# Kernel tuning notes

Hardware: AMD Instinct MI355X
Metric: run time of the kernel (lower is better)

Reference implementation:

```python
import jax, jax.numpy as jnp
import numpy as np

S, B, E, H, FFN = 2048, 2, 1024, 16, 4096
HD = E // H
EPS = 1e-5

def setup_inputs() -> dict:
    key = jax.random.key(0)
    ks = jax.random.split(key, 10)
    w = lambda k, shape: 0.02 * jax.random.normal(k, shape, dtype=jnp.float32)
    inp = {
        "x": jax.random.normal(ks[0], (S, B, E), dtype=jnp.float32),
        "key_padding_mask": jax.random.randint(ks[1], (B, S), 0, 2) == 1,
        # attention projections, stored as (in, out) so y = x @ W + b
        "Wq": w(ks[2], (E, E)), "bq": jnp.zeros((E,), jnp.float32),
        "Wk": w(ks[3], (E, E)), "bk": jnp.zeros((E,), jnp.float32),
        "Wv": w(ks[4], (E, E)), "bv": jnp.zeros((E,), jnp.float32),
        "Wo": w(ks[5], (E, E)), "bo": jnp.zeros((E,), jnp.float32),
        "ln1_g": jnp.ones((E,), jnp.float32), "ln1_b": jnp.zeros((E,), jnp.float32),
        "W1": w(ks[6], (E, FFN)), "b1": jnp.zeros((FFN,), jnp.float32),
        "W2": w(ks[7], (FFN, E)), "b2": jnp.zeros((E,), jnp.float32),
        "ln2_g": jnp.ones((E,), jnp.float32), "ln2_b": jnp.zeros((E,), jnp.float32),
    }
    return inp

def layer_norm(x, g, b):
    m = jnp.mean(x, axis=-1, keepdims=True)
    v = jnp.mean(jnp.square(x - m), axis=-1, keepdims=True)
    return (x - m) * jax.lax.rsqrt(v + EPS) * g + b

def reference(x, key_padding_mask, Wq, bq, Wk, bk, Wv, bv, Wo, bo,
              ln1_g, ln1_b, W1, b1, W2, b2, ln2_g, ln2_b):
    # ---- self-attention (post-LN, normalize_before=False) ----
    residual = x  # (S, B, E)
    scaling = 1.0 / jnp.sqrt(jnp.float32(HD))
    q = (scaling * (x @ Wq + bq)).reshape(S, B, H, HD)
    k = (x @ Wk + bk).reshape(S, B, H, HD)
    v = (x @ Wv + bv).reshape(S, B, H, HD)
    # scores: (B, H, S_q, S_k)
    attn = jnp.einsum('ibhd,jbhd->bhij', q, k)
    attn = jnp.where(key_padding_mask[:, None, None, :], -jnp.inf, attn)
    attn = jax.nn.softmax(attn, axis=-1)
    out = jnp.einsum('bhij,jbhd->ibhd', attn, v).reshape(S, B, E)
    h = out @ Wo + bo
    h = layer_norm(residual + h, ln1_g, ln1_b)
    # ---- FFN ----
    residual = h
    f = jax.nn.relu(h @ W1 + b1) @ W2 + b2
    h = layer_norm(residual + f, ln2_g, ln2_b)
    # torch clamps only when inf/nan appear; finite inputs here so no-op
    return h
```

## Files before the change

kernel.cpp:

```cpp
#include <hip/hip_runtime.h>
#include <hip/hip_bf16.h>

using u16 = unsigned short;
using u32 = unsigned int;

constexpr int S_LEN = 2048, BATCH = 2, EMB = 1024, NHEAD = 16, HDIM = 64, FFN_DIM = 4096;
constexpr int NTOK = S_LEN * BATCH;
constexpr int QKV_N = 3 * EMB;

typedef __attribute__((ext_vector_type(4))) float f32x4;
typedef __attribute__((ext_vector_type(8))) short short8;
typedef __attribute__((ext_vector_type(8))) __bf16 bf16x8;
typedef __attribute__((ext_vector_type(8))) u16 ushort8;
typedef __attribute__((ext_vector_type(4))) u16 u16x4;

typedef const __attribute__((address_space(1))) u16 gu16;
typedef __attribute__((address_space(3))) u16 lu16;

__device__ __forceinline__ u16 f2bf(float f) {
  u32 u = __builtin_bit_cast(u32, f);
  u32 r = u + 0x7fffu + ((u >> 16) & 1u);
  return (u16)(r >> 16);
}
__device__ __forceinline__ float bf2f(u16 u) {
  return __builtin_bit_cast(float, (u32)u << 16);
}

__device__ __forceinline__ f32x4 mfma16(short8 a, short8 b, f32x4 c) {
  return __builtin_amdgcn_mfma_f32_16x16x32_bf16(
      __builtin_bit_cast(bf16x8, a), __builtin_bit_cast(bf16x8, b), c, 0, 0, 0);
}

__device__ __forceinline__ void gload16(const u16* g, u16* l) {
  __builtin_amdgcn_global_load_lds((gu16*)g, (lu16*)l, 16, 0, 0);
}

__global__ __launch_bounds__(256) void k_cvt_bf16(const float* __restrict__ in,
                                                  u16* __restrict__ out, int n) {
  int i = (blockIdx.x * 256 + threadIdx.x) * 8;
  if (i >= n) return;
  float4 a = *(const float4*)(in + i);
  float4 b = *(const float4*)(in + i + 4);
  ushort8 o;
  o[0] = f2bf(a.x); o[1] = f2bf(a.y); o[2] = f2bf(a.z); o[3] = f2bf(a.w);
  o[4] = f2bf(b.x); o[5] = f2bf(b.y); o[6] = f2bf(b.z); o[7] = f2bf(b.w);
  *(ushort8*)(out + i) = o;
}

__global__ __launch_bounds__(256) void k_transpose_w(const float* __restrict__ in,
                                                     u16* __restrict__ out, int R, int C,
                                                     float scale) {
  __shared__ float t[32][33];
  int c0 = blockIdx.x * 32, r0 = blockIdx.y * 32;
  int tx = threadIdx.x & 31, ty = threadIdx.x >> 5;
#pragma unroll
  for (int i = 0; i < 4; ++i)
    t[ty + i * 8][tx] = in[(r0 + ty + i * 8) * C + c0 + tx];
  __syncthreads();
#pragma unroll
  for (int i = 0; i < 4; ++i)
    out[(c0 + ty + i * 8) * R + r0 + tx] = f2bf(t[tx][ty + i * 8] * scale);
}

__global__ void k_bias_cat(const float* __restrict__ bq, const float* __restrict__ bk,
                           const float* __restrict__ bv, float* __restrict__ bcat) {
  int i = blockIdx.x * 256 + threadIdx.x;
  float v = (i < 1024) ? bq[i] * 0.125f : (i < 2048 ? bk[i - 1024] : bv[i - 2048]);
  bcat[i] = v;
}

__global__ void k_transpose_v(const u16* __restrict__ qkvb, u16* __restrict__ vT) {
  __shared__ u16 t[64][65];
  int s0 = blockIdx.x * 64;
  int bh = blockIdx.y;
  int b = bh >> 4, h = bh & 15;
  int tx = threadIdx.x, ty = threadIdx.y;
#pragma unroll
  for (int i = 0; i < 16; ++i) {
    int s = i * 4 + ty;
    t[s][tx] = qkvb[((s0 + s) * BATCH + b) * QKV_N + 2048 + h * HDIM + tx];
  }
  __syncthreads();
#pragma unroll
  for (int i = 0; i < 16; ++i) {
    int d = i * 4 + ty;
    vT[(bh * HDIM + d) * S_LEN + s0 + tx] = t[tx][d];
  }
}

template <int NS, bool RELU>
__global__ __launch_bounds__(256, 4) void k_gemm128(
    const u16* __restrict__ A, const u16* __restrict__ Bt,
    const float* __restrict__ bias, u16* __restrict__ C,
    u16* __restrict__ P1, u16* __restrict__ P2, u16* __restrict__ P3,
    int M, int N, int K, int nbx) {
  __shared__ u16 As[2][128 * 32];
  __shared__ u16 Bs[2][128 * 32];
  int tid = threadIdx.x;
  int lane = tid & 63;
  int lm = lane & 15, lg = lane >> 4;
  int w = tid >> 6;
  int wm = w >> 1, wn = w & 1;

  int cpx = gridDim.x >> 3;
  int nw = (blockIdx.x & 7) * cpx + (blockIdx.x >> 3);
  int nb = gridDim.x / NS;
  int slice = nw / nb;
  int t0 = nw - slice * nb;
  int m0 = (t0 / nbx) * 128, n0 = (t0 % nbx) * 128;
  int klen = K / NS, koff = slice * klen;

  f32x4 z = {0.f, 0.f, 0.f, 0.f};
  f32x4 acc[4][4];
#pragma unroll
  for (int mi = 0; mi < 4; ++mi)
#pragma unroll
    for (int ni = 0; ni < 4; ++ni) acc[mi][ni] = z;

  const u16* aSrc[2];
  const u16* bSrc[2];
  int dOff[2];
#pragma unroll
  for (int i = 0; i < 2; ++i) {
    int ci = i * 256 + tid;
    int row = ci >> 2, ch = ci & 3;
    int sc = 8 * (ch ^ ((row >> 1) & 3));
    aSrc[i] = A + (m0 + row) * K + koff + sc;
    bSrc[i] = Bt + (n0 + row) * K + koff + sc;
    dOff[i] = ci * 8;
  }

  auto stage = [&](int buf, int k0) {
#pragma unroll
    for (int i = 0; i < 2; ++i) {
      gload16(aSrc[i] + k0, &As[buf][0] + dOff[i]);
      gload16(bSrc[i] + k0, &Bs[buf][0] + dOff[i]);
    }
  };

  int swz = (lm >> 1) & 3;
  int nkt = klen >> 5;
  stage(0, 0);
  __syncthreads();
  for (int t = 0; t < nkt; ++t) {
    int cur = t & 1;
    if (t + 1 < nkt) stage(cur ^ 1, (t + 1) << 5);
    const u16* Ab = &As[cur][0];
    const u16* Bb = &Bs[cur][0];
    __builtin_amdgcn_s_setprio(1);
    short8 bf[4];
#pragma unroll
    for (int ni = 0; ni < 4; ++ni) {
      int row = wn * 64 + ni * 16 + lm;
      bf[ni] = *(const short8*)(Bb + row * 32 + 8 * (lg ^ swz));
    }
#pragma unroll
    for (int mi = 0; mi < 4; ++mi) {
      int row = wm * 64 + mi * 16 + lm;
      short8 af = *(const short8*)(Ab + row * 32 + 8 * (lg ^ swz));
#pragma unroll
      for (int ni = 0; ni < 4; ++ni)
        acc[mi][ni] = mfma16(af, bf[ni], acc[mi][ni]);
    }
    __builtin_amdgcn_s_setprio(0);
    __syncthreads();
  }

  u16* Cout = C;
  if (NS > 1) Cout = (slice == 0) ? C : (slice == 1 ? P1 : (slice == 2 ? P2 : P3));
#pragma unroll
  for (int ni = 0; ni < 4; ++ni) {
    int c = n0 + wn * 64 + ni * 16 + lm;
    float bc = (NS == 1) ? bias[c] : 0.f;
#pragma unroll
    for (int mi = 0; mi < 4; ++mi) {
#pragma unroll
      for (int j = 0; j < 4; ++j) {
        int r = m0 + wm * 64 + mi * 16 + lg * 4 + j;
        float x = acc[mi][ni][j] + bc;
        if (RELU) x = fmaxf(x, 0.f);
        Cout[r * N + c] = f2bf(x);
      }
    }
  }
}

template <bool OUTB>
__global__ __launch_bounds__(256) void k_reduce_ln(
    const u16* __restrict__ P0, const u16* __restrict__ P1,
    const u16* __restrict__ P2, const u16* __restrict__ P3,
    const float* __restrict__ bias, const float* __restrict__ resid,
    const float* __restrict__ gam, const float* __restrict__ bet,
    float* __restrict__ outf, u16* __restrict__ outb) {
  int r = blockIdx.x;
  int tid = threadIdx.x;
  int c4 = tid * 4;
  int idx = r * EMB + c4;
  u16x4 a0 = *(const u16x4*)(P0 + idx);
  u16x4 a1 = *(const u16x4*)(P1 + idx);
  u16x4 a2 = *(const u16x4*)(P2 + idx);
  u16x4 a3 = *(const u16x4*)(P3 + idx);
  float4 bi = *(const float4*)(bias + c4);
  float4 rs = *(const float4*)(resid + idx);
  float4 v;
  v.x = bf2f(a0[0]) + bf2f(a1[0]) + bf2f(a2[0]) + bf2f(a3[0]) + bi.x + rs.x;
  v.y = bf2f(a0[1]) + bf2f(a1[1]) + bf2f(a2[1]) + bf2f(a3[1]) + bi.y + rs.y;
  v.z = bf2f(a0[2]) + bf2f(a1[2]) + bf2f(a2[2]) + bf2f(a3[2]) + bi.z + rs.z;
  v.w = bf2f(a0[3]) + bf2f(a1[3]) + bf2f(a2[3]) + bf2f(a3[3]) + bi.w + rs.w;
  float s = v.x + v.y + v.z + v.w;
  float ss = v.x * v.x + v.y * v.y + v.z * v.z + v.w * v.w;
#pragma unroll
  for (int off = 1; off < 64; off <<= 1) {
    s += __shfl_xor(s, off);
    ss += __shfl_xor(ss, off);
  }
  __shared__ float red[2][4];
  int w = tid >> 6, lane = tid & 63;
  if (lane == 0) { red[0][w] = s; red[1][w] = ss; }
  __syncthreads();
  s = red[0][0] + red[0][1] + red[0][2] + red[0][3];
  ss = red[1][0] + red[1][1] + red[1][2] + red[1][3];
  float mean = s * (1.f / EMB);
  float var = ss * (1.f / EMB) - mean * mean;
  float inv = rsqrtf(var + 1e-5f);
  float4 g = *(const float4*)(gam + c4);
  float4 be = *(const float4*)(bet + c4);
  float4 o;
  o.x = (v.x - mean) * inv * g.x + be.x;
  o.y = (v.y - mean) * inv * g.y + be.y;
  o.z = (v.z - mean) * inv * g.z + be.z;
  o.w = (v.w - mean) * inv * g.w + be.w;
  *(float4*)(outf + idx) = o;
  if (OUTB) {
    u16 ob[4] = {f2bf(o.x), f2bf(o.y), f2bf(o.z), f2bf(o.w)};
    *(u16x4*)(outb + idx) = *(u16x4*)ob;
  }
}

__global__ __launch_bounds__(256) void k_attn(
    const u16* __restrict__ qkvb, const u16* __restrict__ vT,
    const int* __restrict__ mask, u16* __restrict__ outb) {
  __shared__ u16 Kl[2][4096];
  __shared__ u16 Vl[2][4096];
  __shared__ u16 Pl[4][1024];
  int tid = threadIdx.x;
  int lane = tid & 63, w = tid >> 6;
  int lm = lane & 15, lg = lane >> 4;
  int L = blockIdx.x;
  int bh = (L & 7) + 8 * (L >> 8);
  int qi0 = ((L >> 3) & 31) * 64;
  int b = bh >> 4, h = bh & 15;

  int qs = qi0 + w * 16 + lm;
  const u16* qp = qkvb + (qs * BATCH + b) * QKV_N + h * HDIM;
  short8 qf0 = *(const short8*)(qp + lg * 8);
  short8 qf1 = *(const short8*)(qp + 32 + lg * 8);

  int r0 = tid >> 3, c8 = tid & 7;
  int swz8 = 8 * (c8 ^ (r0 & 7));
  const u16* kA = qkvb + (r0 * BATCH + b) * QKV_N + 1024 + h * HDIM + swz8;
  const u16* kB = qkvb + ((r0 + 32) * BATCH + b) * QKV_N + 1024 + h * HDIM + swz8;
  const u16* vA = vT + (bh * HDIM + r0) * S_LEN + swz8;
  const u16* vB = vT + (bh * HDIM + r0 + 32) * S_LEN + swz8;
  const int KSTEP = 64 * BATCH * QKV_N;

  const int* mp = mask + b * S_LEN;

  u16* Pw = Pl[w];
  int rd_swz = (lm & 7) << 3;
  const u16* prd0 = Pw + lm * 64 + ((lg * 8) ^ rd_swz);
  const u16* prd1 = Pw + lm * 64 + ((32 + lg * 8) ^ rd_swz);
  int wbase[4], wswz[4];
#pragma unroll
  for (int j = 0; j < 4; ++j) {
    int row = lg * 4 + j;
    wbase[j] = row * 64;
    wswz[j] = (row & 7) << 3;
  }

  f32x4 z = {0.f, 0.f, 0.f, 0.f};
  f32x4 o[4] = {z, z, z, z};
  float lrow[4] = {0.f, 0.f, 0.f, 0.f};
  int mk[4], mknext[4];

  {
    u16* kd = Kl[0] + w * 512;
    u16* vd = Vl[0] + w * 512;
    gload16(kA, kd); gload16(kB, kd + 2048);
    gload16(vA, vd); gload16(vB, vd + 2048);
    kA += KSTEP; kB += KSTEP; vA += 64; vB += 64;
#pragma unroll
    for (int ni = 0; ni < 4; ++ni) mk[ni] = mp[ni * 16 + lm];
  }
  __syncthreads();

  int cur = 0;
  for (int kt = 0; kt < S_LEN; kt += 64) {
    if (kt + 64 < S_LEN) {
      u16* kd = Kl[cur ^ 1] + w * 512;
      u16* vd = Vl[cur ^ 1] + w * 512;
      gload16(kA, kd); gload16(kB, kd + 2048);
      gload16(vA, vd); gload16(vB, vd + 2048);
      kA += KSTEP; kB += KSTEP; vA += 64; vB += 64;
#pragma unroll
      for (int ni = 0; ni < 4; ++ni) mknext[ni] = mp[kt + 64 + ni * 16 + lm];
    }
    const u16* Kc = Kl[cur];
    const u16* Vc = Vl[cur];
#pragma unroll
    for (int ni = 0; ni < 4; ++ni) {
      const u16* kl = Kc + (ni * 16 + lm) * 64;
      short8 k0 = *(const short8*)(kl + ((lg * 8) ^ rd_swz));
      short8 k1 = *(const short8*)(kl + ((32 + lg * 8) ^ rd_swz));
      f32x4 t = mfma16(qf0, k0, z);
      f32x4 sv = mfma16(qf1, k1, t);
      float mb = mk[ni] ? -1e30f : 0.f;
      int csw = ni * 16 + lm;
#pragma unroll
      for (int j = 0; j < 4; ++j) {
        float p = __expf(fminf(sv[j] + mb, 30.f));
        lrow[j] += p;
        Pw[wbase[j] + (csw ^ wswz[j])] = f2bf(p);
      }
    }
    short8 pa0 = *(const short8*)prd0;
    short8 pa1 = *(const short8*)prd1;
#pragma unroll
    for (int ni = 0; ni < 4; ++ni) {
      const u16* vl = Vc + (ni * 16 + lm) * 64;
      short8 v0 = *(const short8*)(vl + ((lg * 8) ^ rd_swz));
      short8 v1 = *(const short8*)(vl + ((32 + lg * 8) ^ rd_swz));
      o[ni] = mfma16(pa0, v0, o[ni]);
      o[ni] = mfma16(pa1, v1, o[ni]);
    }
#pragma unroll
    for (int ni = 0; ni < 4; ++ni) mk[ni] = mknext[ni];
    __syncthreads();
    cur ^= 1;
  }

#pragma unroll
  for (int j = 0; j < 4; ++j) {
    float rs = lrow[j];
    rs += __shfl_xor(rs, 1);
    rs += __shfl_xor(rs, 2);
    rs += __shfl_xor(rs, 4);
    rs += __shfl_xor(rs, 8);
    lrow[j] = 1.f / rs;
  }
#pragma unroll
  for (int ni = 0; ni < 4; ++ni) {
    int c = h * HDIM + ni * 16 + lm;
#pragma unroll
    for (int j = 0; j < 4; ++j) {
      int srow = qi0 + w * 16 + lg * 4 + j;
      outb[(srow * BATCH + b) * EMB + c] = f2bf(o[ni][j] * lrow[j]);
    }
  }
}

extern "C" void kernel_launch(void* const* d_in, const int* in_sizes, int n_in,
                              void* d_out, int out_size, void* d_ws, size_t ws_size,
                              hipStream_t stream) {
  (void)in_sizes; (void)n_in; (void)out_size; (void)ws_size;
  const float* x = (const float*)d_in[0];
  const int* mask = (const int*)d_in[1];
  const float* Wq = (const float*)d_in[2];
  const float* bq = (const float*)d_in[3];
  const float* Wk = (const float*)d_in[4];
  const float* bk = (const float*)d_in[5];
  const float* Wv = (const float*)d_in[6];
  const float* bv = (const float*)d_in[7];
  const float* Wo = (const float*)d_in[8];
  const float* bo = (const float*)d_in[9];
  const float* g1 = (const float*)d_in[10];
  const float* be1 = (const float*)d_in[11];
  const float* W1 = (const float*)d_in[12];
  const float* b1 = (const float*)d_in[13];
  const float* W2 = (const float*)d_in[14];
  const float* b2 = (const float*)d_in[15];
  const float* g2 = (const float*)d_in[16];
  const float* be2 = (const float*)d_in[17];
  float* out = (float*)d_out;

  char* p = (char*)d_ws;
  u16* xb = (u16*)(p);
  u16* WqkvT = (u16*)(p + 8388608);
  u16* WoT = WqkvT + 3 * 1024 * 1024;
  u16* W1T = WoT + 1024 * 1024;
  u16* W2T = W1T + 1024 * 4096;
  u16* qkvb = (u16*)(p + 33554432);
  u16* ao = (u16*)(p + 58720256);
  float* bcat = (float*)(p + 67108864);
  float* hf = (float*)(p + 67108864);
  u16* hb = (u16*)(p + 83886080);
  u16* vT = xb;
  u16* f1b = qkvb;
  u16* PP0 = xb;
  u16* PP1 = hb;
  u16* PP2 = (u16*)(p + 92274688);
  u16* PP3 = (u16*)(p + 100663296);

  k_cvt_bf16<<<NTOK * EMB / 2048, 256, 0, stream>>>(x, xb, NTOK * EMB);
  k_transpose_w<<<dim3(32, 32), 256, 0, stream>>>(Wq, WqkvT, 1024, 1024, 0.125f);
  k_transpose_w<<<dim3(32, 32), 256, 0, stream>>>(Wk, WqkvT + 1024 * 1024, 1024, 1024, 1.f);
  k_transpose_w<<<dim3(32, 32), 256, 0, stream>>>(Wv, WqkvT + 2 * 1024 * 1024, 1024, 1024, 1.f);
  k_transpose_w<<<dim3(32, 32), 256, 0, stream>>>(Wo, WoT, 1024, 1024, 1.f);
  k_transpose_w<<<dim3(128, 32), 256, 0, stream>>>(W1, W1T, 1024, 4096, 1.f);
  k_transpose_w<<<dim3(32, 128), 256, 0, stream>>>(W2, W2T, 4096, 1024, 1.f);
  k_bias_cat<<<12, 256, 0, stream>>>(bq, bk, bv, bcat);

  k_gemm128<1, false><<<(NTOK / 128) * (QKV_N / 128), 256, 0, stream>>>(
      xb, WqkvT, bcat, qkvb, nullptr, nullptr, nullptr, NTOK, QKV_N, EMB, QKV_N / 128);

  k_transpose_v<<<dim3(S_LEN / 64, BATCH * NHEAD), dim3(64, 4), 0, stream>>>(qkvb, vT);
  k_attn<<<1024, 256, 0, stream>>>(qkvb, vT, mask, ao);

  k_gemm128<4, false><<<(NTOK / 128) * (EMB / 128) * 4, 256, 0, stream>>>(
      ao, WoT, nullptr, PP0, PP1, PP2, PP3, NTOK, EMB, EMB, EMB / 128);
  k_reduce_ln<true><<<NTOK, 256, 0, stream>>>(
      PP0, PP1, PP2, PP3, bo, x, g1, be1, hf, hb);

  k_gemm128<1, true><<<(NTOK / 128) * (FFN_DIM / 128), 256, 0, stream>>>(
      hb, W1T, b1, f1b, nullptr, nullptr, nullptr, NTOK, FFN_DIM, EMB, FFN_DIM / 128);

  k_gemm128<4, false><<<(NTOK / 128) * (EMB / 128) * 4, 256, 0, stream>>>(
      f1b, W2T, nullptr, PP0, PP1, PP2, PP3, NTOK, EMB, FFN_DIM, EMB / 128);
  k_reduce_ln<false><<<NTOK, 256, 0, stream>>>(
      PP0, PP1, PP2, PP3, b2, hf, g2, be2, out, nullptr);
}
```

Baseline: 261.0 us.

## Transpose score MFMA, fold log2e into Q scale, pack P stores

The attention score MFMA now uses swapped operands, so each lane holds four consecutive keys for one query row. The mask is precomputed as additive floats and loaded as float4, P values are packed to bf16 with v_cvt_pk_bf16_f32 and written as one 8-byte store, and the row sum becomes a single scalar per lane. Folding log2(e) into the Q scale lets the kernel use exp2 directly. The aim is to cut the per-element exp, convert, scalar LDS store and shuffle work in the inner loop. The cost is an extra small mask kernel and a few shuffles at the end. The maskf buffer sits inside the hf region, but it is consumed before hf is written.

Result: no change. 256.4 us, median of 2 (-1.8%).

```diff
diff --git a/kernel.cpp b/kernel.cpp
--- a/kernel.cpp
+++ b/kernel.cpp
@@ -7,12 +7,14 @@
 constexpr int S_LEN = 2048, BATCH = 2, EMB = 1024, NHEAD = 16, HDIM = 64, FFN_DIM = 4096;
 constexpr int NTOK = S_LEN * BATCH;
 constexpr int QKV_N = 3 * EMB;
+#define QSCALE 0.18033688011112042f
 
 typedef __attribute__((ext_vector_type(4))) float f32x4;
 typedef __attribute__((ext_vector_type(8))) short short8;
 typedef __attribute__((ext_vector_type(8))) __bf16 bf16x8;
 typedef __attribute__((ext_vector_type(8))) u16 ushort8;
 typedef __attribute__((ext_vector_type(4))) u16 u16x4;
+typedef __attribute__((ext_vector_type(2))) u32 u32x2;
 
 typedef const __attribute__((address_space(1))) u16 gu16;
 typedef __attribute__((address_space(3))) u16 lu16;
@@ -33,6 +35,12 @@
 
 __device__ __forceinline__ void gload16(const u16* g, u16* l) {
   __builtin_amdgcn_global_load_lds((gu16*)g, (lu16*)l, 16, 0, 0);
+}
+
+__device__ __forceinline__ u32 cvtpk(float lo, float hi) {
+  u32 r;
+  asm("v_cvt_pk_bf16_f32 %0, %1, %2" : "=v"(r) : "v"(lo), "v"(hi));
+  return r;
 }
 
 __global__ __launch_bounds__(256) void k_cvt_bf16(const float* __restrict__ in,
@@ -65,8 +73,13 @@
 __global__ void k_bias_cat(const float* __restrict__ bq, const float* __restrict__ bk,
                            const float* __restrict__ bv, float* __restrict__ bcat) {
   int i = blockIdx.x * 256 + threadIdx.x;
-  float v = (i < 1024) ? bq[i] * 0.125f : (i < 2048 ? bk[i - 1024] : bv[i - 2048]);
+  float v = (i < 1024) ? bq[i] * QSCALE : (i < 2048 ? bk[i - 1024] : bv[i - 2048]);
   bcat[i] = v;
+}
+
+__global__ void k_mask_f(const int* __restrict__ m, float* __restrict__ mf, int n) {
+  int i = blockIdx.x * 256 + threadIdx.x;
+  if (i < n) mf[i] = m[i] ? -1e30f : 0.f;
 }
 
 __global__ void k_transpose_v(const u16* __restrict__ qkvb, u16* __restrict__ vT) {
@@ -239,7 +252,7 @@
 
 __global__ __launch_bounds__(256) void k_attn(
     const u16* __restrict__ qkvb, const u16* __restrict__ vT,
-    const int* __restrict__ mask, u16* __restrict__ outb) {
+    const float* __restrict__ maskf, u16* __restrict__ outb) {
   __shared__ u16 Kl[2][4096];
   __shared__ u16 Vl[2][4096];
   __shared__ u16 Pl[4][1024];
@@ -264,24 +277,21 @@
   const u16* vB = vT + (bh * HDIM + r0 + 32) * S_LEN + swz8;
   const int KSTEP = 64 * BATCH * QKV_N;
 
-  const int* mp = mask + b * S_LEN;
+  const float* mp = maskf + b * S_LEN;
 
   u16* Pw = Pl[w];
   int rd_swz = (lm & 7) << 3;
   const u16* prd0 = Pw + lm * 64 + ((lg * 8) ^ rd_swz);
   const u16* prd1 = Pw + lm * 64 + ((32 + lg * 8) ^ rd_swz);
-  int wbase[4], wswz[4];
-#pragma unroll
-  for (int j = 0; j < 4; ++j) {
-    int row = lg * 4 + j;
-    wbase[j] = row * 64;
-    wswz[j] = (row & 7) << 3;
-  }
+  u16* pwr[4];
+#pragma unroll
+  for (int ni = 0; ni < 4; ++ni)
+    pwr[ni] = Pw + lm * 64 + ((ni * 16 + lg * 4) ^ rd_swz);
 
   f32x4 z = {0.f, 0.f, 0.f, 0.f};
   f32x4 o[4] = {z, z, z, z};
-  float lrow[4] = {0.f, 0.f, 0.f, 0.f};
-  int mk[4], mknext[4];
+  float lrow = 0.f;
+  float4 mk[4], mknext[4];
 
   {
     u16* kd = Kl[0] + w * 512;
@@ -290,7 +300,8 @@
     gload16(vA, vd); gload16(vB, vd + 2048);
     kA += KSTEP; kB += KSTEP; vA += 64; vB += 64;
 #pragma unroll
-    for (int ni = 0; ni < 4; ++ni) mk[ni] = mp[ni * 16 + lm];
+    for (int ni = 0; ni < 4; ++ni)
+      mk[ni] = *(const float4*)(mp + ni * 16 + lg * 4);
   }
   __syncthreads();
 
@@ -303,7 +314,8 @@
       gload16(vA, vd); gload16(vB, vd + 2048);
       kA += KSTEP; kB += KSTEP; vA += 64; vB += 64;
 #pragma unroll
-      for (int ni = 0; ni < 4; ++ni) mknext[ni] = mp[kt + 64 + ni * 16 + lm];
+      for (int ni = 0; ni < 4; ++ni)
+        mknext[ni] = *(const float4*)(mp + kt + 64 + ni * 16 + lg * 4);
     }
     const u16* Kc = Kl[cur];
     const u16* Vc = Vl[cur];
@@ -312,16 +324,18 @@
       const u16* kl = Kc + (ni * 16 + lm) * 64;
       short8 k0 = *(const short8*)(kl + ((lg * 8) ^ rd_swz));
       short8 k1 = *(const short8*)(kl + ((32 + lg * 8) ^ rd_swz));
-      f32x4 t = mfma16(qf0, k0, z);
-      f32x4 sv = mfma16(qf1, k1, t);
-      float mb = mk[ni] ? -1e30f : 0.f;
-      int csw = ni * 16 + lm;
-#pragma unroll
-      for (int j = 0; j < 4; ++j) {
-        float p = __expf(fminf(sv[j] + mb, 30.f));
-        lrow[j] += p;
-        Pw[wbase[j] + (csw ^ wswz[j])] = f2bf(p);
-      }
+      f32x4 t = mfma16(k0, qf0, z);
+      f32x4 sv = mfma16(k1, qf1, t);
+      float4 mb = mk[ni];
+      float p0 = __builtin_amdgcn_exp2f(fminf(sv[0] + mb.x, 42.f));
+      float p1 = __builtin_amdgcn_exp2f(fminf(sv[1] + mb.y, 42.f));
+      float p2 = __builtin_amdgcn_exp2f(fminf(sv[2] + mb.z, 42.f));
+      float p3 = __builtin_amdgcn_exp2f(fminf(sv[3] + mb.w, 42.f));
+      lrow += (p0 + p1) + (p2 + p3);
+      u32x2 pk;
+      pk[0] = cvtpk(p0, p1);
+      pk[1] = cvtpk(p2, p3);
+      *(u32x2*)pwr[ni] = pk;
     }
     short8 pa0 = *(const short8*)prd0;
     short8 pa1 = *(const short8*)prd1;
@@ -339,22 +353,20 @@
     cur ^= 1;
   }
 
-#pragma unroll
-  for (int j = 0; j < 4; ++j) {
-    float rs = lrow[j];
-    rs += __shfl_xor(rs, 1);
-    rs += __shfl_xor(rs, 2);
-    rs += __shfl_xor(rs, 4);
-    rs += __shfl_xor(rs, 8);
-    lrow[j] = 1.f / rs;
-  }
+  lrow += __shfl_xor(lrow, 16);
+  lrow += __shfl_xor(lrow, 32);
+  float inv = 1.f / lrow;
+  float invj[4];
+#pragma unroll
+  for (int j = 0; j < 4; ++j) invj[j] = __shfl(inv, lg * 4 + j);
+
 #pragma unroll
   for (int ni = 0; ni < 4; ++ni) {
     int c = h * HDIM + ni * 16 + lm;
 #pragma unroll
     for (int j = 0; j < 4; ++j) {
       int srow = qi0 + w * 16 + lg * 4 + j;
-      outb[(srow * BATCH + b) * EMB + c] = f2bf(o[ni][j] * lrow[j]);
+      outb[(srow * BATCH + b) * EMB + c] = f2bf(o[ni][j] * invj[j]);
     }
   }
 }
@@ -392,6 +404,7 @@
   u16* qkvb = (u16*)(p + 33554432);
   u16* ao = (u16*)(p + 58720256);
   float* bcat = (float*)(p + 67108864);
+  float* maskf = (float*)(p + 67108864 + 16384);
   float* hf = (float*)(p + 67108864);
   u16* hb = (u16*)(p + 83886080);
   u16* vT = xb;
@@ -402,19 +415,20 @@
   u16* PP3 = (u16*)(p + 100663296);
 
   k_cvt_bf16<<<NTOK * EMB / 2048, 256, 0, stream>>>(x, xb, NTOK * EMB);
-  k_transpose_w<<<dim3(32, 32), 256, 0, stream>>>(Wq, WqkvT, 1024, 1024, 0.125f);
+  k_transpose_w<<<dim3(32, 32), 256, 0, stream>>>(Wq, WqkvT, 1024, 1024, QSCALE);
   k_transpose_w<<<dim3(32, 32), 256, 0, stream>>>(Wk, WqkvT + 1024 * 1024, 1024, 1024, 1.f);
   k_transpose_w<<<dim3(32, 32), 256, 0, stream>>>(Wv, WqkvT + 2 * 1024 * 1024, 1024, 1024, 1.f);
   k_transpose_w<<<dim3(32, 32), 256, 0, stream>>>(Wo, WoT, 1024, 1024, 1.f);
   k_transpose_w<<<dim3(128, 32), 256, 0, stream>>>(W1, W1T, 1024, 4096, 1.f);
   k_transpose_w<<<dim3(32, 128), 256, 0, stream>>>(W2, W2T, 4096, 1024, 1.f);
   k_bias_cat<<<12, 256, 0, stream>>>(bq, bk, bv, bcat);
+  k_mask_f<<<16, 256, 0, stream>>>(mask, maskf, BATCH * S_LEN);
 
   k_gemm128<1, false><<<(NTOK / 128) * (QKV_N / 128), 256, 0, stream>>>(
       xb, WqkvT, bcat, qkvb, nullptr, nullptr, nullptr, NTOK, QKV_N, EMB, QKV_N / 128);
 
   k_transpose_v<<<dim3(S_LEN / 64, BATCH * NHEAD), dim3(64, 4), 0, stream>>>(qkvb, vT);
-  k_attn<<<1024, 256, 0, stream>>>(qkvb, vT, mask, ao);
+  k_attn<<<1024, 256, 0, stream>>>(qkvb, vT, maskf, ao);
 
   k_gemm128<4, false><<<(NTOK / 128) * (EMB / 128) * 4, 256, 0, stream>>>(
       ao, WoT, nullptr, PP0, PP1, PP2, PP3, NTOK, EMB, EMB, EMB / 128);
```
